# Optimization experiments

Measured on AMD Instinct MI355X. Metric: run time of the kernel, lower is better.

Reference implementation:

```python
import jax, jax.numpy as jnp
import numpy as np


def setup_inputs() -> dict:
    key = jax.random.key(0)
    k1, k2, k3, k4, k5 = jax.random.split(key, 5)
    B, S, D, U = 64, 2048, 512, 512
    he = lambda k, shape: jax.random.normal(k, shape, dtype=jnp.float32) * jnp.sqrt(2.0 / shape[0])
    return {
        "query": jax.random.normal(k1, (B, D), dtype=jnp.float32),
        "values": jax.random.normal(k2, (B, S, D), dtype=jnp.float32),
        "W1": he(k3, (D, U)),
        "W2": he(k4, (D, U)),
        "V1": he(k5, (U, 1)),
    }


def reference(query, values, W1, W2, V1):
    # query: (B, D), values: (B, S, D)
    Q = query @ W1                       # (B, U)
    V = jnp.einsum("bsd,du->bsu", values, W2)  # (B, S, U)
    add = jnp.tanh(Q[:, None, :] + V)    # (B, S, U)
    score = jnp.einsum("bsu,uo->bso", add, V1)  # (B, S, 1)
    attn = jax.nn.softmax(score, axis=1)         # (B, S, 1)
    context = jnp.sum(attn * values, axis=1)     # (B, D)
    return context
```

## Files before the change

### kernel.cpp

```cpp
#include <hip/hip_runtime.h>


typedef __attribute__((ext_vector_type(8))) short bf16x8;
typedef __attribute__((ext_vector_type(4))) float f32x4;

#if __has_builtin(__builtin_amdgcn_exp2f)
__device__ __forceinline__ float fast_exp2(float x) { return __builtin_amdgcn_exp2f(x); }
#else
__device__ __forceinline__ float fast_exp2(float x) { return exp2f(x); }
#endif
#if __has_builtin(__builtin_amdgcn_rcpf)
__device__ __forceinline__ float fast_rcp(float x) { return __builtin_amdgcn_rcpf(x); }
#else
__device__ __forceinline__ float fast_rcp(float x) { return 1.0f / x; }
#endif

__device__ __forceinline__ unsigned short f2bf(float f) {
  unsigned int u = __float_as_uint(f);
  u += 0x7fffu + ((u >> 16) & 1u);
  return (unsigned short)(u >> 16);
}

__global__ void qk(const float* __restrict__ query, const float* __restrict__ W1,
                   float* __restrict__ Q) {
  __shared__ float qrow[512];
  const int b = blockIdx.x, half = blockIdx.y, t = threadIdx.x;
  qrow[t] = query[b * 512 + t];
  qrow[t + 256] = query[b * 512 + t + 256];
  __syncthreads();
  const int u = half * 256 + t;
  float acc = 0.f;
#pragma unroll 8
  for (int k = 0; k < 512; ++k) acc += qrow[k] * W1[(size_t)k * 512 + u];
  Q[b * 512 + u] = acc;
}

__global__ void wt_k(const float* __restrict__ W2, unsigned short* __restrict__ Wt) {
  __shared__ float tile[32][33];
  const int k0 = blockIdx.x * 32, n0 = blockIdx.y * 32;
  const int tx = threadIdx.x, ty = threadIdx.y;
  for (int i = 0; i < 32; i += 8)
    tile[ty + i][tx] = W2[(size_t)(k0 + ty + i) * 512 + n0 + tx];
  __syncthreads();
  for (int i = 0; i < 32; i += 8)
    Wt[(size_t)(n0 + ty + i) * 512 + k0 + tx] = f2bf(tile[tx][ty + i]);
}

__global__ __launch_bounds__(512, 4) void scores_k(
    const float* __restrict__ values, const unsigned short* __restrict__ Wt,
    const float* __restrict__ Q, const float* __restrict__ V1,
    float* __restrict__ scores) {
  __shared__ __align__(16) unsigned short Ab[64 * 512];
  __shared__ float sAcc[64];

  const int t = threadIdx.x;
  const int lane = t & 63;
  const int w = t >> 6;
  const int quad = lane >> 4;
  const int l15 = lane & 15;
  const int m0 = blockIdx.x * 64;
  const int b = m0 >> 11;

  if (t < 64) sAcc[t] = 0.0f;

  const float* Ag = values + (size_t)m0 * 512;
#pragma unroll
  for (int i = 0; i < 8; ++i) {
    const int c = i * 512 + t;
    const int m = c >> 6;
    const int kc = c & 63;
    const float4* src = (const float4*)(Ag + (size_t)m * 512 + kc * 8);
    const float4 x = src[0], y = src[1];
    const unsigned int p0 = (unsigned int)f2bf(x.x) | ((unsigned int)f2bf(x.y) << 16);
    const unsigned int p1 = (unsigned int)f2bf(x.z) | ((unsigned int)f2bf(x.w) << 16);
    const unsigned int p2 = (unsigned int)f2bf(y.x) | ((unsigned int)f2bf(y.y) << 16);
    const unsigned int p3 = (unsigned int)f2bf(y.z) | ((unsigned int)f2bf(y.w) << 16);
    *(uint4*)&Ab[m * 512 + ((kc ^ (m & 7)) * 8)] = make_uint4(p0, p1, p2, p3);
  }
  __syncthreads();

  f32x4 acc[4][4];
#pragma unroll
  for (int mt = 0; mt < 4; ++mt)
#pragma unroll
    for (int nt = 0; nt < 4; ++nt) acc[mt][nt] = (f32x4){0.f, 0.f, 0.f, 0.f};

  const unsigned short* Bg = Wt + (size_t)(w * 64 + l15) * 512 + quad * 8;
  const int sw = l15 & 7;

#pragma unroll
  for (int ks = 0; ks < 16; ++ks) {
    bf16x8 bfr[4], af[4];
#pragma unroll
    for (int nt = 0; nt < 4; ++nt)
      bfr[nt] = *(const bf16x8*)(Bg + nt * (16 * 512) + ks * 32);
#pragma unroll
    for (int mt = 0; mt < 4; ++mt) {
      const int m = mt * 16 + l15;
      af[mt] = *(const bf16x8*)&Ab[m * 512 + (((ks * 4 + quad) ^ sw) * 8)];
    }
#pragma unroll
    for (int mt = 0; mt < 4; ++mt)
#pragma unroll
      for (int nt = 0; nt < 4; ++nt)
        acc[mt][nt] = __builtin_amdgcn_mfma_f32_16x16x32_bf16(af[mt], bfr[nt],
                                                              acc[mt][nt], 0, 0, 0);
  }

  float part[4][4];
#pragma unroll
  for (int mt = 0; mt < 4; ++mt)
#pragma unroll
    for (int r = 0; r < 4; ++r) part[mt][r] = 0.f;

#pragma unroll
  for (int nt = 0; nt < 4; ++nt) {
    const int n = w * 64 + nt * 16 + l15;
    const float qv = Q[b * 512 + n];
    const float v1 = V1[n];
#pragma unroll
    for (int mt = 0; mt < 4; ++mt)
#pragma unroll
      for (int r = 0; r < 4; ++r) {
        const float x = acc[mt][nt][r] + qv;
        const float e = fast_exp2(x * 2.8853900817779268f);
        const float th = 1.0f - 2.0f * fast_rcp(e + 1.0f);
        part[mt][r] += th * v1;
      }
  }
#pragma unroll
  for (int mt = 0; mt < 4; ++mt)
#pragma unroll
    for (int r = 0; r < 4; ++r) {
      float v = part[mt][r];
      v += __shfl_xor(v, 1);
      v += __shfl_xor(v, 2);
      v += __shfl_xor(v, 4);
      v += __shfl_xor(v, 8);
      if (l15 == 0) atomicAdd(&sAcc[mt * 16 + quad * 4 + r], v);
    }
  __syncthreads();
  if (t < 64) scores[m0 + t] = sAcc[t];
}

__global__ void softmax_k(float* __restrict__ scores, float* __restrict__ out) {
  __shared__ float red[8];
  const int bq = blockIdx.x, t = threadIdx.x;
  out[bq * 512 + t] = 0.f;
  out[bq * 512 + 256 + t] = 0.f;
  float* s = scores + (size_t)bq * 2048;
  float v[8];
  float mx = -3.0e38f;
#pragma unroll
  for (int i = 0; i < 8; ++i) {
    v[i] = s[t + i * 256];
    mx = fmaxf(mx, v[i]);
  }
#pragma unroll
  for (int o = 1; o < 64; o <<= 1) mx = fmaxf(mx, __shfl_xor(mx, o));
  if ((t & 63) == 0) red[t >> 6] = mx;
  __syncthreads();
  mx = fmaxf(fmaxf(red[0], red[1]), fmaxf(red[2], red[3]));
  float e[8];
  float sum = 0.f;
#pragma unroll
  for (int i = 0; i < 8; ++i) {
    e[i] = fast_exp2((v[i] - mx) * 1.4426950408889634f);
    sum += e[i];
  }
#pragma unroll
  for (int o = 1; o < 64; o <<= 1) sum += __shfl_xor(sum, o);
  if ((t & 63) == 0) red[4 + (t >> 6)] = sum;
  __syncthreads();
  const float inv = 1.0f / (red[4] + red[5] + red[6] + red[7]);
#pragma unroll
  for (int i = 0; i < 8; ++i) s[t + i * 256] = e[i] * inv;
}

__global__ __launch_bounds__(512) void ctx_k(const float* __restrict__ values,
                                             const float* __restrict__ attn,
                                             float* __restrict__ out) {
  const int bid = blockIdx.x;
  const int b = bid >> 3, sc = bid & 7;
  const int t = threadIdx.x;
  const float* vb = values + (size_t)b * 2048 * 512 + (size_t)sc * 256 * 512;
  const float* ab = attn + (size_t)b * 2048 + sc * 256;
  float acc = 0.f;
#pragma unroll 8
  for (int s = 0; s < 256; ++s) acc += ab[s] * vb[(size_t)s * 512 + t];
  atomicAdd(&out[b * 512 + t], acc);
}

extern "C" void kernel_launch(void* const* d_in, const int* in_sizes, int n_in,
                              void* d_out, int out_size, void* d_ws, size_t ws_size,
                              hipStream_t stream) {
  const float* query = (const float*)d_in[0];
  const float* values = (const float*)d_in[1];
  const float* W1 = (const float*)d_in[2];
  const float* W2 = (const float*)d_in[3];
  const float* V1 = (const float*)d_in[4];
  float* out = (float*)d_out;

  char* ws = (char*)d_ws;
  float* Qp = (float*)ws;
  unsigned short* Wtp = (unsigned short*)(ws + 131072);
  float* Sp = (float*)(ws + 131072 + 524288);

  qk<<<dim3(64, 2), 256, 0, stream>>>(query, W1, Qp);
  wt_k<<<dim3(16, 16), dim3(32, 8), 0, stream>>>(W2, Wtp);
  scores_k<<<2048, 512, 0, stream>>>(values, Wtp, Qp, V1, Sp);
  softmax_k<<<64, 256, 0, stream>>>(Sp, out);
  ctx_k<<<512, 512, 0, stream>>>(values, Sp, out);
}
```

Baseline: 528.6 us.

## Pre-swizzle W2 into MFMA fragment order and fuse softmax into context kernel

The W2 transpose kernel now writes bf16 weights directly in per-lane MFMA B-fragment order, so each lane's B loads in the scores kernel become contiguous 16-byte reads across the wavefront. The same kernel also zeroes the output. The separate softmax kernel is removed. Each context block recomputes the max and sum over its batch's 2048 scores and normalises its own 256-score chunk in shared memory, which saves one launch and a global round trip at the cost of redundant reductions across the 8 blocks per batch.

```diff
diff --git a/kernel.cpp b/kernel.cpp
--- a/kernel.cpp
+++ b/kernel.cpp
@@ -35,19 +35,28 @@
   Q[b * 512 + u] = acc;
 }
 
-__global__ void wt_k(const float* __restrict__ W2, unsigned short* __restrict__ Wt) {
-  __shared__ float tile[32][33];
-  const int k0 = blockIdx.x * 32, n0 = blockIdx.y * 32;
-  const int tx = threadIdx.x, ty = threadIdx.y;
-  for (int i = 0; i < 32; i += 8)
-    tile[ty + i][tx] = W2[(size_t)(k0 + ty + i) * 512 + n0 + tx];
-  __syncthreads();
-  for (int i = 0; i < 32; i += 8)
-    Wt[(size_t)(n0 + ty + i) * 512 + k0 + tx] = f2bf(tile[tx][ty + i]);
+__global__ void wt_k(const float* __restrict__ W2, unsigned short* __restrict__ Wtf,
+                     float* __restrict__ out0) {
+  const int gid = blockIdx.x * 256 + threadIdx.x;
+  out0[gid] = 0.f;
+  const int lane = gid & 63;
+  const int g = gid >> 6;
+  const int ks = g & 15, ntile = g >> 4;
+  const int l15 = lane & 15, quad = lane >> 4;
+  const int n = ntile * 16 + l15;
+  const int k0 = ks * 32 + quad * 8;
+  unsigned int p[4];
+#pragma unroll
+  for (int jj = 0; jj < 4; ++jj) {
+    const float a = W2[(size_t)(k0 + 2 * jj) * 512 + n];
+    const float b = W2[(size_t)(k0 + 2 * jj + 1) * 512 + n];
+    p[jj] = (unsigned int)f2bf(a) | ((unsigned int)f2bf(b) << 16);
+  }
+  *(uint4*)&Wtf[(size_t)gid * 8] = make_uint4(p[0], p[1], p[2], p[3]);
 }
 
 __global__ __launch_bounds__(512, 4) void scores_k(
-    const float* __restrict__ values, const unsigned short* __restrict__ Wt,
+    const float* __restrict__ values, const unsigned short* __restrict__ Wtf,
     const float* __restrict__ Q, const float* __restrict__ V1,
     float* __restrict__ scores) {
   __shared__ __align__(16) unsigned short Ab[64 * 512];
@@ -85,7 +94,7 @@
 #pragma unroll
     for (int nt = 0; nt < 4; ++nt) acc[mt][nt] = (f32x4){0.f, 0.f, 0.f, 0.f};
 
-  const unsigned short* Bg = Wt + (size_t)(w * 64 + l15) * 512 + quad * 8;
+  const unsigned short* Bg = Wtf + (size_t)lane * 8;
   const int sw = l15 & 7;
 
 #pragma unroll
@@ -93,7 +102,7 @@
     bf16x8 bfr[4], af[4];
 #pragma unroll
     for (int nt = 0; nt < 4; ++nt)
-      bfr[nt] = *(const bf16x8*)(Bg + nt * (16 * 512) + ks * 32);
+      bfr[nt] = *(const bf16x8*)(Bg + (size_t)((w * 4 + nt) * 16 + ks) * 512);
 #pragma unroll
     for (int mt = 0; mt < 4; ++mt) {
       const int m = mt * 16 + l15;
@@ -143,51 +152,39 @@
   if (t < 64) scores[m0 + t] = sAcc[t];
 }
 
-__global__ void softmax_k(float* __restrict__ scores, float* __restrict__ out) {
-  __shared__ float red[8];
-  const int bq = blockIdx.x, t = threadIdx.x;
-  out[bq * 512 + t] = 0.f;
-  out[bq * 512 + 256 + t] = 0.f;
-  float* s = scores + (size_t)bq * 2048;
-  float v[8];
-  float mx = -3.0e38f;
-#pragma unroll
-  for (int i = 0; i < 8; ++i) {
-    v[i] = s[t + i * 256];
-    mx = fmaxf(mx, v[i]);
-  }
-#pragma unroll
-  for (int o = 1; o < 64; o <<= 1) mx = fmaxf(mx, __shfl_xor(mx, o));
-  if ((t & 63) == 0) red[t >> 6] = mx;
-  __syncthreads();
-  mx = fmaxf(fmaxf(red[0], red[1]), fmaxf(red[2], red[3]));
-  float e[8];
-  float sum = 0.f;
-#pragma unroll
-  for (int i = 0; i < 8; ++i) {
-    e[i] = fast_exp2((v[i] - mx) * 1.4426950408889634f);
-    sum += e[i];
-  }
-#pragma unroll
-  for (int o = 1; o < 64; o <<= 1) sum += __shfl_xor(sum, o);
-  if ((t & 63) == 0) red[4 + (t >> 6)] = sum;
-  __syncthreads();
-  const float inv = 1.0f / (red[4] + red[5] + red[6] + red[7]);
-#pragma unroll
-  for (int i = 0; i < 8; ++i) s[t + i * 256] = e[i] * inv;
-}
-
 __global__ __launch_bounds__(512) void ctx_k(const float* __restrict__ values,
-                                             const float* __restrict__ attn,
+                                             const float* __restrict__ scores,
                                              float* __restrict__ out) {
+  __shared__ float red[16];
+  __shared__ float wsc[256];
   const int bid = blockIdx.x;
   const int b = bid >> 3, sc = bid & 7;
   const int t = threadIdx.x;
-  const float* vb = values + (size_t)b * 2048 * 512 + (size_t)sc * 256 * 512;
-  const float* ab = attn + (size_t)b * 2048 + sc * 256;
+  const float* sb = scores + (size_t)b * 2048;
+  const float v0 = sb[t], v1 = sb[t + 512], v2 = sb[t + 1024], v3 = sb[t + 1536];
+  float mx = fmaxf(fmaxf(v0, v1), fmaxf(v2, v3));
+#pragma unroll
+  for (int o = 1; o < 64; o <<= 1) mx = fmaxf(mx, __shfl_xor(mx, o));
+  if ((t & 63) == 0) red[t >> 6] = mx;
+  __syncthreads();
+  mx = fmaxf(fmaxf(fmaxf(red[0], red[1]), fmaxf(red[2], red[3])),
+             fmaxf(fmaxf(red[4], red[5]), fmaxf(red[6], red[7])));
+  const float L2E = 1.4426950408889634f;
+  float sum = fast_exp2((v0 - mx) * L2E) + fast_exp2((v1 - mx) * L2E) +
+              fast_exp2((v2 - mx) * L2E) + fast_exp2((v3 - mx) * L2E);
+#pragma unroll
+  for (int o = 1; o < 64; o <<= 1) sum += __shfl_xor(sum, o);
+  if ((t & 63) == 0) red[8 + (t >> 6)] = sum;
+  __syncthreads();
+  sum = (red[8] + red[9]) + (red[10] + red[11]) + (red[12] + red[13]) +
+        (red[14] + red[15]);
+  const float inv = 1.0f / sum;
+  if (t < 256) wsc[t] = fast_exp2((sb[sc * 256 + t] - mx) * L2E) * inv;
+  __syncthreads();
+  const float* vb = values + ((size_t)b * 2048 + sc * 256) * 512;
   float acc = 0.f;
 #pragma unroll 8
-  for (int s = 0; s < 256; ++s) acc += ab[s] * vb[(size_t)s * 512 + t];
+  for (int s = 0; s < 256; ++s) acc += wsc[s] * vb[(size_t)s * 512 + t];
   atomicAdd(&out[b * 512 + t], acc);
 }
 
@@ -207,8 +204,7 @@
   float* Sp = (float*)(ws + 131072 + 524288);
 
   qk<<<dim3(64, 2), 256, 0, stream>>>(query, W1, Qp);
-  wt_k<<<dim3(16, 16), dim3(32, 8), 0, stream>>>(W2, Wtp);
+  wt_k<<<128, 256, 0, stream>>>(W2, Wtp, out);
   scores_k<<<2048, 512, 0, stream>>>(values, Wtp, Qp, V1, Sp);
-  softmax_k<<<64, 256, 0, stream>>>(Sp, out);
   ctx_k<<<512, 512, 0, stream>>>(values, Sp, out);
 }
```

Measured after the change: 498.9 us. 1.06x faster.
